# Kernel optimization log

Measured on AMD Instinct MI355X. Metric: run time of the kernel, lower is better.

The kernel has to match this reference:

```python
import jax, jax.numpy as jnp
import numpy as np

N, E = 20000, 320000
IN_DIM, HID, OUT_DIM, HEADS = 128, 64, 64, 4


def _lin_params(key, fan_in, fan_out):
    kw, kb = jax.random.split(key)
    s = 1.0 / np.sqrt(fan_in)
    W = jax.random.uniform(kw, (fan_in, fan_out), jnp.float32, -s, s)
    b = jax.random.uniform(kb, (fan_out,), jnp.float32, -s, s)
    return W, b


def setup_inputs() -> dict:
    key = jax.random.key(0)
    ks = jax.random.split(key, 12)
    x = jax.random.normal(ks[0], (N, IN_DIM), jnp.float32)
    edge_index = jax.random.randint(ks[1], (2, E), 0, N, jnp.int64)
    W1, b1 = _lin_params(ks[2], IN_DIM, HID)
    # conv1: in=HID, per-head out=HID, heads=HEADS, concat=True
    Wq1, bq1 = _lin_params(ks[3], HID, HID * HEADS)
    Wk1, bk1 = _lin_params(ks[4], HID, HID * HEADS)
    Wv1, bv1 = _lin_params(ks[5], HID, HID * HEADS)
    Ws1, bs1 = _lin_params(ks[6], HID, HID * HEADS)
    # conv2: in=HID*HEADS, out=OUT_DIM, heads=1, concat=False
    Wq2, bq2 = _lin_params(ks[7], HID * HEADS, OUT_DIM)
    Wk2, bk2 = _lin_params(ks[8], HID * HEADS, OUT_DIM)
    Wv2, bv2 = _lin_params(ks[9], HID * HEADS, OUT_DIM)
    Ws2, bs2 = _lin_params(ks[10], HID * HEADS, OUT_DIM)
    return dict(x=x, edge_index=edge_index, W1=W1, b1=b1,
                Wq1=Wq1, bq1=bq1, Wk1=Wk1, bk1=bk1, Wv1=Wv1, bv1=bv1, Ws1=Ws1, bs1=bs1,
                Wq2=Wq2, bq2=bq2, Wk2=Wk2, bk2=bk2, Wv2=Wv2, bv2=bv2, Ws2=Ws2, bs2=bs2)


def transformer_conv(x, src, dst, Wq, bq, Wk, bk, Wv, bv, Ws, bs, heads, concat):
    n = x.shape[0]
    c = Wq.shape[1] // heads  # per-head channels
    q = (x @ Wq + bq).reshape(n, heads, c)
    k = (x @ Wk + bk).reshape(n, heads, c)
    v = (x @ Wv + bv).reshape(n, heads, c)
    # per-edge attention logits, grouped-by-dst softmax
    alpha = jnp.einsum('ehc,ehc->eh', q[dst], k[src]) / jnp.sqrt(jnp.float32(c))
    m = jax.ops.segment_max(alpha, dst, num_segments=n)  # [n, heads]
    m = jnp.where(jnp.isfinite(m), m, 0.0)
    ex = jnp.exp(alpha - m[dst])
    denom = jax.ops.segment_sum(ex, dst, num_segments=n)
    a = ex / (denom[dst] + 1e-16)  # [E, heads]
    out = jax.ops.segment_sum(a[..., None] * v[src], dst, num_segments=n)  # [n, heads, c]
    out = out.reshape(n, heads * c) if concat else out.mean(axis=1)
    return out + (x @ Ws + bs)  # root/skip connection


def reference(x, edge_index, W1, b1, Wq1, bq1, Wk1, bk1, Wv1, bv1, Ws1, bs1,
              Wq2, bq2, Wk2, bk2, Wv2, bv2, Ws2, bs2):
    src, dst = edge_index[0], edge_index[1]
    h = jax.nn.relu(x @ W1 + b1)
    h = transformer_conv(h, src, dst, Wq1, bq1, Wk1, bk1, Wv1, bv1, Ws1, bs1, HEADS, True)
    h = jax.nn.relu(h)  # dropout is identity in eval mode
    out = transformer_conv(h, src, dst, Wq2, bq2, Wk2, bk2, Wv2, bv2, Ws2, bs2, 1, False)
    return out
```

## Files before the change

kernel.cpp:

```cpp
#include <hip/hip_runtime.h>
#include <hip/hip_bf16.h>
#include <math.h>

typedef short short8 __attribute__((ext_vector_type(8)));
typedef float f32x4 __attribute__((ext_vector_type(4)));
typedef float f32x2 __attribute__((ext_vector_type(2)));

__device__ __forceinline__ unsigned short pk_bf16(float x) {
    unsigned int b = __float_as_uint(x);
    b += 0x7fffu + ((b >> 16) & 1u);
    return (unsigned short)(b >> 16);
}
__device__ __forceinline__ void unpack8(const uint4 u, float* f) {
    f[0] = __uint_as_float(u.x << 16); f[1] = __uint_as_float(u.x & 0xffff0000u);
    f[2] = __uint_as_float(u.y << 16); f[3] = __uint_as_float(u.y & 0xffff0000u);
    f[4] = __uint_as_float(u.z << 16); f[5] = __uint_as_float(u.z & 0xffff0000u);
    f[6] = __uint_as_float(u.w << 16); f[7] = __uint_as_float(u.w & 0xffff0000u);
}
__device__ __forceinline__ unsigned char enc_fp8(float x) {
    return (unsigned char)(__builtin_amdgcn_cvt_pk_fp8_f32(x, x, 0, false) & 0xff);
}
__device__ __forceinline__ void unpack8_fp8(const uint2 u, float* f) {
    f32x2 a = __builtin_amdgcn_cvt_pk_f32_fp8(u.x, false);
    f32x2 b = __builtin_amdgcn_cvt_pk_f32_fp8(u.x, true);
    f32x2 c = __builtin_amdgcn_cvt_pk_f32_fp8(u.y, false);
    f32x2 d = __builtin_amdgcn_cvt_pk_f32_fp8(u.y, true);
    f[0] = a.x; f[1] = a.y; f[2] = b.x; f[3] = b.y;
    f[4] = c.x; f[5] = c.y; f[6] = d.x; f[7] = d.y;
}
__device__ __forceinline__ float qsum4(float x) {
    x += __int_as_float(__builtin_amdgcn_mov_dpp(__float_as_int(x), 0xB1, 0xF, 0xF, true));
    x += __int_as_float(__builtin_amdgcn_mov_dpp(__float_as_int(x), 0x4E, 0xF, 0xF, true));
    return x;
}

__global__ void count_kernel(const int* __restrict__ dst, int* __restrict__ deg, int E) {
    int e = blockIdx.x * blockDim.x + threadIdx.x;
    if (e < E) atomicAdd(&deg[dst[e]], 1);
}

__global__ __launch_bounds__(1024) void scanA_kernel(const int* __restrict__ deg,
                                                     int* __restrict__ offs,
                                                     int* __restrict__ bsum, int n) {
    __shared__ int s[1024];
    const int i = blockIdx.x * 1024 + threadIdx.x;
    const int v = (i < n) ? deg[i] : 0;
    s[threadIdx.x] = v;
    __syncthreads();
    for (int off = 1; off < 1024; off <<= 1) {
        int t = (threadIdx.x >= off) ? s[threadIdx.x - off] : 0;
        __syncthreads();
        s[threadIdx.x] += t;
        __syncthreads();
    }
    if (i < n) offs[i] = s[threadIdx.x] - v;
    if (threadIdx.x == 1023) bsum[blockIdx.x] = s[1023];
}

__global__ void scanB_kernel(const int* __restrict__ bsum, int* __restrict__ bpre, int nb) {
    const int t = threadIdx.x;
    int v = (t < nb) ? bsum[t] : 0;
    const int orig = v;
    for (int off = 1; off < 64; off <<= 1) {
        int o = __shfl_up(v, off, 64);
        if (t >= off) v += o;
    }
    if (t < nb) bpre[t] = v - orig;
    if (t == 63) bpre[nb] = v;
}

__global__ __launch_bounds__(1024) void scanC_kernel(int* __restrict__ offs,
                                                     int* __restrict__ cursor,
                                                     const int* __restrict__ bpre,
                                                     int n, int nb) {
    const int i = blockIdx.x * 1024 + threadIdx.x;
    if (i < n) {
        const int o = offs[i] + bpre[blockIdx.x];
        offs[i] = o;
        cursor[i] = o;
    }
    if (i == 0) offs[n] = bpre[nb];
}

__global__ void fill_kernel(const int* __restrict__ src, const int* __restrict__ dst,
                            int* __restrict__ cursor, int* __restrict__ csrc, int E) {
    int e = blockIdx.x * blockDim.x + threadIdx.x;
    if (e < E) {
        int p = atomicAdd(&cursor[dst[e]], 1);
        csrc[p] = src[e];
    }
}

template <int K, int NT, int CFG>
__device__ __forceinline__ void convw_body(const float* Wa, const float* Wb,
                                           const float* Wc, const float* Wd,
                                           unsigned short* out, int t) {
    constexpr int KS = K / 32;
    if (t >= NT * K * 64) return;
    const int jj = t & 7;
    const int lane = (t >> 3) & 63;
    const int nf = (t >> 9) & 3;
    const int rest = t >> 11;
    const int ks = rest % KS;
    const int nt = rest / KS;
    const int k = ks * 32 + (lane >> 4) * 8 + jj;
    const int c64 = nf * 16 + (lane & 15);
    float v;
    if (CFG == 1) {
        const int j = nt >> 2;
        const float* W = (j == 0) ? Wa : (j == 1) ? Wb : (j == 2) ? Wc : Wd;
        v = W[(size_t)k * 256 + (nt & 3) * 64 + c64];
    } else if (CFG == 2) {
        const float* W = (nt == 0) ? Wa : (nt == 1) ? Wb : (nt == 2) ? Wc : Wd;
        v = W[(size_t)k * 64 + c64];
    } else {
        v = Wa[(size_t)k * 64 + c64];
    }
    out[t] = pk_bf16(v);
}

__global__ __launch_bounds__(256) void prep_kernel(
    const float* __restrict__ x, unsigned short* __restrict__ xb, int nx, int nA,
    const float* __restrict__ W1, unsigned short* __restrict__ wswzL,
    const float* __restrict__ Wq1, const float* __restrict__ Wk1,
    const float* __restrict__ Wv1, const float* __restrict__ Ws1,
    unsigned short* __restrict__ wswz1,
    const float* __restrict__ Wq2, const float* __restrict__ Wk2,
    const float* __restrict__ Wv2, const float* __restrict__ Ws2,
    unsigned short* __restrict__ wswz2) {
    int b = blockIdx.x;
    if (b < nA) {
        int t = b * 256 + threadIdx.x;
        if (t < nx) xb[t] = pk_bf16(x[t]);
        return;
    }
    b -= nA;
    if (b < 32) { convw_body<128, 1, 0>(W1, W1, W1, W1, wswzL, b * 256 + threadIdx.x); return; }
    b -= 32;
    if (b < 256) { convw_body<64, 16, 1>(Wq1, Wk1, Wv1, Ws1, wswz1, b * 256 + threadIdx.x); return; }
    b -= 256;
    convw_body<256, 4, 2>(Wq2, Wk2, Wv2, Ws2, wswz2, b * 256 + threadIdx.x);
}

template <int K, int NT, int KIND>
__global__ __launch_bounds__(256) void mfma_gemm_kernel(
    const unsigned short* __restrict__ A, const unsigned short* __restrict__ Wswz,
    const float* __restrict__ ba, const float* __restrict__ bb,
    const float* __restrict__ bc, const float* __restrict__ bd,
    unsigned short* __restrict__ qout, unsigned char* __restrict__ kvout,
    void* __restrict__ sout, unsigned short* __restrict__ hout, int n) {
    constexpr int KS = K / 32;
    const int nt = blockIdx.x;
    const int w = threadIdx.x >> 6, l = threadIdx.x & 63;
    const int r0 = blockIdx.y * 64 + w * 16;
    const int lrow = l & 15, lk = l >> 4;

    f32x4 acc[4] = {};
    const unsigned short* wp = Wswz + (size_t)nt * KS * 4 * 512 + (size_t)l * 8;
    const unsigned short* ap = A + (size_t)(r0 + lrow) * K + lk * 8;

#pragma unroll
    for (int ks = 0; ks < KS; ++ks) {
        const short8 a = *(const short8*)(ap + ks * 32);
        const short8 b0 = *(const short8*)(wp + (ks * 4 + 0) * 512);
        const short8 b1 = *(const short8*)(wp + (ks * 4 + 1) * 512);
        const short8 b2 = *(const short8*)(wp + (ks * 4 + 2) * 512);
        const short8 b3 = *(const short8*)(wp + (ks * 4 + 3) * 512);
        acc[0] = __builtin_amdgcn_mfma_f32_16x16x32_bf16(a, b0, acc[0], 0, 0, 0);
        acc[1] = __builtin_amdgcn_mfma_f32_16x16x32_bf16(a, b1, acc[1], 0, 0, 0);
        acc[2] = __builtin_amdgcn_mfma_f32_16x16x32_bf16(a, b2, acc[2], 0, 0, 0);
        acc[3] = __builtin_amdgcn_mfma_f32_16x16x32_bf16(a, b3, acc[3], 0, 0, 0);
    }

    const int colg = l & 15, rowg = l >> 4;
#pragma unroll
    for (int nf = 0; nf < 4; ++nf) {
        const int c64 = nf * 16 + colg;
        float bias;
        if (KIND == 0) {
            bias = ba[c64];
        } else if (KIND == 1) {
            const int j = nt >> 2;
            const float* bsel = (j == 0) ? ba : (j == 1) ? bb : (j == 2) ? bc : bd;
            bias = bsel[(nt & 3) * 64 + c64];
        } else {
            const float* bsel = (nt == 0) ? ba : (nt == 1) ? bb : (nt == 2) ? bc : bd;
            bias = bsel[c64];
        }
#pragma unroll
        for (int r = 0; r < 4; ++r) {
            const int row = r0 + rowg * 4 + r;
            if (row >= n) continue;
            const float val = acc[nf][r] + bias;
            if (KIND == 0) {
                hout[(size_t)row * 64 + c64] = pk_bf16(fmaxf(val, 0.f));
            } else if (KIND == 1) {
                const int j = nt >> 2, hd = nt & 3;
                if (j == 0) {
                    qout[(size_t)row * 256 + hd * 64 + c64] = pk_bf16(val);
                } else if (j == 1) {
                    kvout[((size_t)row * 4 + hd) * 192 + c64] = enc_fp8(val);
                } else if (j == 2) {
                    *(unsigned short*)(kvout + ((size_t)row * 4 + hd) * 192 + 64 + c64 * 2) =
                        pk_bf16(val);
                } else {
                    ((unsigned short*)sout)[(size_t)row * 256 + hd * 64 + c64] = pk_bf16(val);
                }
            } else {
                if (nt == 0) {
                    qout[(size_t)row * 64 + c64] = pk_bf16(val);
                } else if (nt == 1) {
                    kvout[(size_t)row * 192 + c64] = enc_fp8(val);
                } else if (nt == 2) {
                    *(unsigned short*)(kvout + (size_t)row * 192 + 64 + c64 * 2) = pk_bf16(val);
                } else {
                    ((float*)sout)[(size_t)row * 64 + c64] = val;
                }
            }
        }
    }
}

__global__ __launch_bounds__(256) void attn4_kernel(
    const unsigned short* __restrict__ q, const unsigned char* __restrict__ kv,
    const unsigned short* __restrict__ s,
    const int* __restrict__ offs, const int* __restrict__ csrc,
    unsigned short* __restrict__ out, int n) {
    const int head = threadIdx.x >> 6;
    const int lane = threadIdx.x & 63;
    const int g = lane >> 3;
    const int sl = lane & 7;
    const int node = blockIdx.x;
    if (node >= n) return;
    const unsigned colbase = (head << 6) + (sl << 3);
    const unsigned koff = head * 192 + sl * 8;
    const unsigned voff = head * 192 + 64 + sl * 16;

    float qv[8];
    {
        uint4 qu = *(const uint4*)(q + ((unsigned)node << 8) + colbase);
        unpack8(qu, qv);
        const float qs = 0.125f * 1.44269504f;
#pragma unroll
        for (int i = 0; i < 8; ++i) qv[i] *= qs;
    }

    const int e0 = offs[node], e1 = offs[node + 1];
    float denom = 0.f;
    float acc[8] = {0.f, 0.f, 0.f, 0.f, 0.f, 0.f, 0.f, 0.f};

    int e = e0 + g;
    bool valid = e < e1;
    uint2 ku; uint4 vu;
    if (valid) {
        const unsigned char* kvp = kv + (size_t)(unsigned)csrc[e] * 768;
        ku = *(const uint2*)(kvp + koff);
        vu = *(const uint4*)(kvp + voff);
    }
    int en = e + 8;
    bool vn = en < e1;
    int srcn = vn ? csrc[en] : 0;

    while (valid) {
        uint2 kun; uint4 vun;
        if (vn) {
            const unsigned char* kvp = kv + (size_t)(unsigned)srcn * 768;
            kun = *(const uint2*)(kvp + koff);
            vun = *(const uint4*)(kvp + voff);
        }
        const int en2 = en + 8;
        const bool vn2 = en2 < e1;
        const int srcn2 = vn2 ? csrc[en2] : 0;

        float kf[8], vf[8];
        unpack8_fp8(ku, kf); unpack8(vu, vf);
        float dot = qv[0] * kf[0] + qv[1] * kf[1] + qv[2] * kf[2] + qv[3] * kf[3]
                  + qv[4] * kf[4] + qv[5] * kf[5] + qv[6] * kf[6] + qv[7] * kf[7];
        dot = qsum4(dot);
        dot += __shfl_xor(dot, 4, 64);
        const float wgt = __builtin_amdgcn_exp2f(dot);
#pragma unroll
        for (int i = 0; i < 8; ++i) acc[i] = fmaf(wgt, vf[i], acc[i]);
        denom += wgt;

        valid = vn; vn = vn2;
        en = en2; srcn = srcn2;
        ku = kun; vu = vun;
    }

#pragma unroll
    for (int off = 8; off <= 32; off <<= 1) {
        denom += __shfl_xor(denom, off, 64);
#pragma unroll
        for (int i = 0; i < 8; ++i) acc[i] += __shfl_xor(acc[i], off, 64);
    }

    if (g == 0) {
        float sv[8];
        uint4 su = *(const uint4*)(s + ((unsigned)node << 8) + colbase);
        unpack8(su, sv);
        const float inv = 1.f / (denom + 1e-16f);
        uint4 p;
        unsigned r[8];
#pragma unroll
        for (int i = 0; i < 8; ++i) r[i] = pk_bf16(fmaxf(acc[i] * inv + sv[i], 0.f));
        p.x = r[0] | (r[1] << 16);
        p.y = r[2] | (r[3] << 16);
        p.z = r[4] | (r[5] << 16);
        p.w = r[6] | (r[7] << 16);
        *(uint4*)(out + ((unsigned)node << 8) + colbase) = p;
    }
}

__global__ __launch_bounds__(256) void attn1_kernel(
    const unsigned short* __restrict__ q, const unsigned char* __restrict__ kv,
    const float* __restrict__ s,
    const int* __restrict__ offs, const int* __restrict__ csrc,
    float* __restrict__ out, int n) {
    const int w = threadIdx.x >> 6;
    const int lane = threadIdx.x & 63;
    const int g = lane >> 3;
    const int sl = lane & 7;
    const int node = blockIdx.x * 4 + w;
    if (node >= n) return;
    const unsigned koff = sl * 8;
    const unsigned voff = 64 + sl * 16;

    float qv[8];
    {
        uint4 qu = *(const uint4*)(q + ((unsigned)node << 6) + (sl << 3));
        unpack8(qu, qv);
        const float qs = 0.125f * 1.44269504f;
#pragma unroll
        for (int i = 0; i < 8; ++i) qv[i] *= qs;
    }

    const int e0 = offs[node], e1 = offs[node + 1];
    float denom = 0.f;
    float acc[8] = {0.f, 0.f, 0.f, 0.f, 0.f, 0.f, 0.f, 0.f};

    int e = e0 + g;
    bool valid = e < e1;
    uint2 ku; uint4 vu;
    if (valid) {
        const unsigned char* kvp = kv + (size_t)(unsigned)csrc[e] * 192;
        ku = *(const uint2*)(kvp + koff);
        vu = *(const uint4*)(kvp + voff);
    }
    int en = e + 8;
    bool vn = en < e1;
    int srcn = vn ? csrc[en] : 0;

    while (valid) {
        uint2 kun; uint4 vun;
        if (vn) {
            const unsigned char* kvp = kv + (size_t)(unsigned)srcn * 192;
            kun = *(const uint2*)(kvp + koff);
            vun = *(const uint4*)(kvp + voff);
        }
        const int en2 = en + 8;
        const bool vn2 = en2 < e1;
        const int srcn2 = vn2 ? csrc[en2] : 0;

        float kf[8], vf[8];
        unpack8_fp8(ku, kf); unpack8(vu, vf);
        float dot = qv[0] * kf[0] + qv[1] * kf[1] + qv[2] * kf[2] + qv[3] * kf[3]
                  + qv[4] * kf[4] + qv[5] * kf[5] + qv[6] * kf[6] + qv[7] * kf[7];
        dot = qsum4(dot);
        dot += __shfl_xor(dot, 4, 64);
        const float wgt = __builtin_amdgcn_exp2f(dot);
#pragma unroll
        for (int i = 0; i < 8; ++i) acc[i] = fmaf(wgt, vf[i], acc[i]);
        denom += wgt;

        valid = vn; vn = vn2;
        en = en2; srcn = srcn2;
        ku = kun; vu = vun;
    }

#pragma unroll
    for (int off = 8; off <= 32; off <<= 1) {
        denom += __shfl_xor(denom, off, 64);
#pragma unroll
        for (int i = 0; i < 8; ++i) acc[i] += __shfl_xor(acc[i], off, 64);
    }

    if (g == 0) {
        const float* sp = s + ((unsigned)node << 6) + (sl << 3);
        const float4 sva = *(const float4*)sp;
        const float4 svb = *(const float4*)(sp + 4);
        const float inv = 1.f / (denom + 1e-16f);
        float4 oa, ob;
        oa.x = acc[0] * inv + sva.x; oa.y = acc[1] * inv + sva.y;
        oa.z = acc[2] * inv + sva.z; oa.w = acc[3] * inv + sva.w;
        ob.x = acc[4] * inv + svb.x; ob.y = acc[5] * inv + svb.y;
        ob.z = acc[6] * inv + svb.z; ob.w = acc[7] * inv + svb.w;
        float* op = out + ((unsigned)node << 6) + (sl << 3);
        *(float4*)op = oa;
        *(float4*)(op + 4) = ob;
    }
}

extern "C" void kernel_launch(void* const* d_in, const int* in_sizes, int n_in,
                              void* d_out, int out_size, void* d_ws, size_t ws_size,
                              hipStream_t stream) {
    const float* x   = (const float*)d_in[0];
    const int*   ei  = (const int*)d_in[1];
    const float* W1  = (const float*)d_in[2];
    const float* b1  = (const float*)d_in[3];
    const float* Wq1 = (const float*)d_in[4];  const float* bq1 = (const float*)d_in[5];
    const float* Wk1 = (const float*)d_in[6];  const float* bk1 = (const float*)d_in[7];
    const float* Wv1 = (const float*)d_in[8];  const float* bv1 = (const float*)d_in[9];
    const float* Ws1 = (const float*)d_in[10]; const float* bs1 = (const float*)d_in[11];
    const float* Wq2 = (const float*)d_in[12]; const float* bq2 = (const float*)d_in[13];
    const float* Wk2 = (const float*)d_in[14]; const float* bk2 = (const float*)d_in[15];
    const float* Wv2 = (const float*)d_in[16]; const float* bv2 = (const float*)d_in[17];
    const float* Ws2 = (const float*)d_in[18]; const float* bs2 = (const float*)d_in[19];

    const int N = in_sizes[0] / 128;
    const int E = in_sizes[1] / 2;
    const int* srcv = ei;
    const int* dstv = ei + E;
    const int rowgroups = (N + 63) / 64;
    const int Mpad = rowgroups * 64;
    const int nscan = (N + 1023) / 1024;

    char* p = (char*)d_ws;
    auto alloc = [&](size_t bytes) -> void* {
        void* r = (void*)p;
        p += (bytes + 255) & ~(size_t)255;
        return r;
    };
    unsigned short* xb  = (unsigned short*)alloc((size_t)Mpad * 128 * 2);
    unsigned short* h1b = (unsigned short*)alloc((size_t)Mpad * 64 * 2);
    unsigned short* q1b = (unsigned short*)alloc((size_t)N * 256 * 2);
    unsigned char*  kv1 = (unsigned char*)alloc((size_t)N * 4 * 192);
    unsigned short* s1b = (unsigned short*)alloc((size_t)N * 256 * 2);
    unsigned short* h2b = (unsigned short*)alloc((size_t)Mpad * 256 * 2);
    unsigned short* q2b = (unsigned short*)alloc((size_t)N * 64 * 2);
    unsigned char*  kv2 = (unsigned char*)alloc((size_t)N * 192);
    float* s2 = (float*)alloc((size_t)N * 64 * 4);
    unsigned short* wswzL = (unsigned short*)alloc((size_t)1 * 128 * 64 * 2);
    unsigned short* wswz1 = (unsigned short*)alloc((size_t)16 * 64 * 64 * 2);
    unsigned short* wswz2 = (unsigned short*)alloc((size_t)4 * 256 * 64 * 2);
    int* deg    = (int*)alloc((size_t)N * 4);
    int* offs   = (int*)alloc(((size_t)N + 1) * 4);
    int* cursor = (int*)alloc((size_t)N * 4);
    int* csrc   = (int*)alloc((size_t)E * 4);
    int* bsum   = (int*)alloc((size_t)(nscan + 1) * 4);
    int* bpre   = (int*)alloc((size_t)(nscan + 1) * 4);
    (void)ws_size; (void)n_in; (void)out_size;

    hipMemsetAsync(deg, 0, (size_t)N * 4, stream);
    count_kernel<<<(E + 255) / 256, 256, 0, stream>>>(dstv, deg, E);
    scanA_kernel<<<nscan, 1024, 0, stream>>>(deg, offs, bsum, N);
    scanB_kernel<<<1, 64, 0, stream>>>(bsum, bpre, nscan);
    scanC_kernel<<<nscan, 1024, 0, stream>>>(offs, cursor, bpre, N, nscan);
    fill_kernel<<<(E + 255) / 256, 256, 0, stream>>>(srcv, dstv, cursor, csrc, E);

    const int nx = N * 128;
    const int nA = (nx + 255) / 256;
    prep_kernel<<<nA + 32 + 256 + 256, 256, 0, stream>>>(
        x, xb, nx, nA, W1, wswzL, Wq1, Wk1, Wv1, Ws1, wswz1, Wq2, Wk2, Wv2, Ws2, wswz2);

    mfma_gemm_kernel<128, 1, 0><<<dim3(1, rowgroups), 256, 0, stream>>>(
        xb, wswzL, b1, b1, b1, b1, nullptr, nullptr, nullptr, h1b, N);

    mfma_gemm_kernel<64, 16, 1><<<dim3(16, rowgroups), 256, 0, stream>>>(
        h1b, wswz1, bq1, bk1, bv1, bs1, q1b, kv1, (void*)s1b, nullptr, N);

    attn4_kernel<<<N, 256, 0, stream>>>(q1b, kv1, s1b, offs, csrc, h2b, N);

    mfma_gemm_kernel<256, 4, 2><<<dim3(4, rowgroups), 256, 0, stream>>>(
        h2b, wswz2, bq2, bk2, bv2, bs2, q2b, kv2, (void*)s2, nullptr, N);

    attn1_kernel<<<(N + 3) / 4, 256, 0, stream>>>(q2b, kv2, s2, offs, csrc,
                                                  (float*)d_out, N);
}
```

Measured before the change: 154.6 us.

## Fuse CSR-build kernels, merge first linear into fill, remap attn4 blocks by head

Folds the deg memset into the prep kernel and replaces the three-kernel scan with a single scan in which each block recomputes its prefix base by summing all earlier degrees. The first linear layer now runs inside the same launch as the CSR fill, which drops several launches and lets those two independent pieces of work overlap. attn4 now gives each block four nodes for one head, with blocks interleaved so that adjacent blocks cover the same head, which changes gather locality. The trade-off is redundant global reads of deg in the scan, since later blocks re-read nearly the whole array.

```diff
diff --git a/kernel.cpp b/kernel.cpp
--- a/kernel.cpp
+++ b/kernel.cpp
@@ -39,56 +39,38 @@
     if (e < E) atomicAdd(&deg[dst[e]], 1);
 }
 
-__global__ __launch_bounds__(1024) void scanA_kernel(const int* __restrict__ deg,
-                                                     int* __restrict__ offs,
-                                                     int* __restrict__ bsum, int n) {
+__global__ __launch_bounds__(1024) void scan_kernel(const int* __restrict__ deg,
+                                                    int* __restrict__ offs,
+                                                    int* __restrict__ cursor,
+                                                    int n, int nb) {
     __shared__ int s[1024];
-    const int i = blockIdx.x * 1024 + threadIdx.x;
+    const int b = blockIdx.x, t = threadIdx.x;
+    int partial = 0;
+    for (int i = t; i < b * 1024; i += 1024) partial += deg[i];
+    s[t] = partial;
+    __syncthreads();
+    for (int off = 512; off > 0; off >>= 1) {
+        if (t < off) s[t] += s[t + off];
+        __syncthreads();
+    }
+    const int base = s[0];
+    __syncthreads();
+    const int i = b * 1024 + t;
     const int v = (i < n) ? deg[i] : 0;
-    s[threadIdx.x] = v;
+    s[t] = v;
     __syncthreads();
     for (int off = 1; off < 1024; off <<= 1) {
-        int t = (threadIdx.x >= off) ? s[threadIdx.x - off] : 0;
+        int x = (t >= off) ? s[t - off] : 0;
         __syncthreads();
-        s[threadIdx.x] += t;
+        s[t] += x;
         __syncthreads();
     }
-    if (i < n) offs[i] = s[threadIdx.x] - v;
-    if (threadIdx.x == 1023) bsum[blockIdx.x] = s[1023];
-}
-
-__global__ void scanB_kernel(const int* __restrict__ bsum, int* __restrict__ bpre, int nb) {
-    const int t = threadIdx.x;
-    int v = (t < nb) ? bsum[t] : 0;
-    const int orig = v;
-    for (int off = 1; off < 64; off <<= 1) {
-        int o = __shfl_up(v, off, 64);
-        if (t >= off) v += o;
-    }
-    if (t < nb) bpre[t] = v - orig;
-    if (t == 63) bpre[nb] = v;
-}
-
-__global__ __launch_bounds__(1024) void scanC_kernel(int* __restrict__ offs,
-                                                     int* __restrict__ cursor,
-                                                     const int* __restrict__ bpre,
-                                                     int n, int nb) {
-    const int i = blockIdx.x * 1024 + threadIdx.x;
     if (i < n) {
-        const int o = offs[i] + bpre[blockIdx.x];
+        const int o = base + s[t] - v;
         offs[i] = o;
         cursor[i] = o;
     }
-    if (i == 0) offs[n] = bpre[nb];
-}
-
-__global__ void fill_kernel(const int* __restrict__ src, const int* __restrict__ dst,
-                            int* __restrict__ cursor, int* __restrict__ csrc, int E) {
-    int e = blockIdx.x * blockDim.x + threadIdx.x;
-    if (e < E) {
-        int p = atomicAdd(&cursor[dst[e]], 1);
-        csrc[p] = src[e];
-    }
+    if (b == nb - 1 && t == 1023) offs[n] = base + s[1023];
 }
 
 template <int K, int NT, int CFG>
@@ -127,7 +109,8 @@
     unsigned short* __restrict__ wswz1,
     const float* __restrict__ Wq2, const float* __restrict__ Wk2,
     const float* __restrict__ Wv2, const float* __restrict__ Ws2,
-    unsigned short* __restrict__ wswz2) {
+    unsigned short* __restrict__ wswz2,
+    int* __restrict__ deg, int ndeg) {
     int b = blockIdx.x;
     if (b < nA) {
         int t = b * 256 + threadIdx.x;
@@ -139,7 +122,12 @@
     b -= 32;
     if (b < 256) { convw_body<64, 16, 1>(Wq1, Wk1, Wv1, Ws1, wswz1, b * 256 + threadIdx.x); return; }
     b -= 256;
-    convw_body<256, 4, 2>(Wq2, Wk2, Wv2, Ws2, wswz2, b * 256 + threadIdx.x);
+    if (b < 256) { convw_body<256, 4, 2>(Wq2, Wk2, Wv2, Ws2, wswz2, b * 256 + threadIdx.x); return; }
+    b -= 256;
+    {
+        int t = b * 256 + threadIdx.x;
+        if (t < ndeg) deg[t] = 0;
+    }
 }
 
 template <int K, int NT, int KIND>
@@ -148,7 +136,7 @@
     const float* __restrict__ ba, const float* __restrict__ bb,
     const float* __restrict__ bc, const float* __restrict__ bd,
     unsigned short* __restrict__ qout, unsigned char* __restrict__ kvout,
-    void* __restrict__ sout, unsigned short* __restrict__ hout, int n) {
+    void* __restrict__ sout, int n) {
     constexpr int KS = K / 32;
     const int nt = blockIdx.x;
     const int w = threadIdx.x >> 6, l = threadIdx.x & 63;
@@ -177,9 +165,7 @@
     for (int nf = 0; nf < 4; ++nf) {
         const int c64 = nf * 16 + colg;
         float bias;
-        if (KIND == 0) {
-            bias = ba[c64];
-        } else if (KIND == 1) {
+        if (KIND == 1) {
             const int j = nt >> 2;
             const float* bsel = (j == 0) ? ba : (j == 1) ? bb : (j == 2) ? bc : bd;
             bias = bsel[(nt & 3) * 64 + c64];
@@ -192,9 +178,7 @@
             const int row = r0 + rowg * 4 + r;
             if (row >= n) continue;
             const float val = acc[nf][r] + bias;
-            if (KIND == 0) {
-                hout[(size_t)row * 64 + c64] = pk_bf16(fmaxf(val, 0.f));
-            } else if (KIND == 1) {
+            if (KIND == 1) {
                 const int j = nt >> 2, hd = nt & 3;
                 if (j == 0) {
                     qout[(size_t)row * 256 + hd * 64 + c64] = pk_bf16(val);
@@ -221,17 +205,75 @@
     }
 }
 
+__device__ __forceinline__ void lin_body(const unsigned short* __restrict__ A,
+                                         const unsigned short* __restrict__ Wswz,
+                                         const float* __restrict__ bias,
+                                         unsigned short* __restrict__ hout,
+                                         int n, int by, int tid) {
+    constexpr int K = 128, KS = 4;
+    const int w = tid >> 6, l = tid & 63;
+    const int r0 = by * 64 + w * 16;
+    const int lrow = l & 15, lk = l >> 4;
+
+    f32x4 acc[4] = {};
+    const unsigned short* wp = Wswz + (size_t)l * 8;
+    const unsigned short* ap = A + (size_t)(r0 + lrow) * K + lk * 8;
+
+#pragma unroll
+    for (int ks = 0; ks < KS; ++ks) {
+        const short8 a = *(const short8*)(ap + ks * 32);
+        const short8 b0 = *(const short8*)(wp + (ks * 4 + 0) * 512);
+        const short8 b1 = *(const short8*)(wp + (ks * 4 + 1) * 512);
+        const short8 b2 = *(const short8*)(wp + (ks * 4 + 2) * 512);
+        const short8 b3 = *(const short8*)(wp + (ks * 4 + 3) * 512);
+        acc[0] = __builtin_amdgcn_mfma_f32_16x16x32_bf16(a, b0, acc[0], 0, 0, 0);
+        acc[1] = __builtin_amdgcn_mfma_f32_16x16x32_bf16(a, b1, acc[1], 0, 0, 0);
+        acc[2] = __builtin_amdgcn_mfma_f32_16x16x32_bf16(a, b2, acc[2], 0, 0, 0);
+        acc[3] = __builtin_amdgcn_mfma_f32_16x16x32_bf16(a, b3, acc[3], 0, 0, 0);
+    }
+    const int colg = l & 15, rowg = l >> 4;
+#pragma unroll
+    for (int nf = 0; nf < 4; ++nf) {
+        const int c64 = nf * 16 + colg;
+        const float bias_v = bias[c64];
+#pragma unroll
+        for (int r = 0; r < 4; ++r) {
+            const int row = r0 + rowg * 4 + r;
+            if (row >= n) continue;
+            hout[(size_t)row * 64 + c64] = pk_bf16(fmaxf(acc[nf][r] + bias_v, 0.f));
+        }
+    }
+}
+
+__global__ __launch_bounds__(256) void fill_lin_kernel(
+    const int* __restrict__ src, const int* __restrict__ dst,
+    int* __restrict__ cursor, int* __restrict__ csrc, int E, int nfill,
+    const unsigned short* __restrict__ xb, const unsigned short* __restrict__ wswzL,
+    const float* __restrict__ b1, unsigned short* __restrict__ h1b, int n) {
+    if ((int)blockIdx.x < nfill) {
+        int e = blockIdx.x * 256 + threadIdx.x;
+        if (e < E) {
+            int p = atomicAdd(&cursor[dst[e]], 1);
+            csrc[p] = src[e];
+        }
+        return;
+    }
+    lin_body(xb, wswzL, b1, h1b, n, blockIdx.x - nfill, threadIdx.x);
+}
+
 __global__ __launch_bounds__(256) void attn4_kernel(
     const unsigned short* __restrict__ q, const unsigned char* __restrict__ kv,
     const unsigned short* __restrict__ s,
     const int* __restrict__ offs, const int* __restrict__ csrc,
     unsigned short* __restrict__ out, int n) {
-    const int head = threadIdx.x >> 6;
+    const int bid = blockIdx.x;
+    const int head = (bid & 7) >> 1;
+    const int ng = (bid >> 3) * 2 + (bid & 1);
     const int lane = threadIdx.x & 63;
+    const int node = ng * 4 + (threadIdx.x >> 6);
+    if (node >= n) return;
     const int g = lane >> 3;
     const int sl = lane & 7;
-    const int node = blockIdx.x;
-    if (node >= n) return;
     const unsigned colbase = (head << 6) + (sl << 3);
     const unsigned koff = head * 192 + sl * 8;
     const unsigned voff = head * 192 + 64 + sl * 16;
@@ -447,32 +489,32 @@
     int* offs   = (int*)alloc(((size_t)N + 1) * 4);
     int* cursor = (int*)alloc((size_t)N * 4);
     int* csrc   = (int*)alloc((size_t)E * 4);
-    int* bsum   = (int*)alloc((size_t)(nscan + 1) * 4);
-    int* bpre   = (int*)alloc((size_t)(nscan + 1) * 4);
     (void)ws_size; (void)n_in; (void)out_size;
-
-    hipMemsetAsync(deg, 0, (size_t)N * 4, stream);
-    count_kernel<<<(E + 255) / 256, 256, 0, stream>>>(dstv, deg, E);
-    scanA_kernel<<<nscan, 1024, 0, stream>>>(deg, offs, bsum, N);
-    scanB_kernel<<<1, 64, 0, stream>>>(bsum, bpre, nscan);
-    scanC_kernel<<<nscan, 1024, 0, stream>>>(offs, cursor, bpre, N, nscan);
-    fill_kernel<<<(E + 255) / 256, 256, 0, stream>>>(srcv, dstv, cursor, csrc, E);
 
     const int nx = N * 128;
     const int nA = (nx + 255) / 256;
-    prep_kernel<<<nA + 32 + 256 + 256, 256, 0, stream>>>(
-        x, xb, nx, nA, W1, wswzL, Wq1, Wk1, Wv1, Ws1, wswz1, Wq2, Wk2, Wv2, Ws2, wswz2);
-
-    mfma_gemm_kernel<128, 1, 0><<<dim3(1, rowgroups), 256, 0, stream>>>(
-        xb, wswzL, b1, b1, b1, b1, nullptr, nullptr, nullptr, h1b, N);
+    const int nZ = (N + 255) / 256;
+    prep_kernel<<<nA + 32 + 256 + 256 + nZ, 256, 0, stream>>>(
+        x, xb, nx, nA, W1, wswzL, Wq1, Wk1, Wv1, Ws1, wswz1,
+        Wq2, Wk2, Wv2, Ws2, wswz2, deg, N);
+
+    count_kernel<<<(E + 255) / 256, 256, 0, stream>>>(dstv, deg, E);
+
+    scan_kernel<<<nscan, 1024, 0, stream>>>(deg, offs, cursor, N, nscan);
+
+    const int nfill = (E + 255) / 256;
+    fill_lin_kernel<<<nfill + rowgroups, 256, 0, stream>>>(
+        srcv, dstv, cursor, csrc, E, nfill, xb, wswzL, b1, h1b, N);
 
     mfma_gemm_kernel<64, 16, 1><<<dim3(16, rowgroups), 256, 0, stream>>>(
-        h1b, wswz1, bq1, bk1, bv1, bs1, q1b, kv1, (void*)s1b, nullptr, N);
-
-    attn4_kernel<<<N, 256, 0, stream>>>(q1b, kv1, s1b, offs, csrc, h2b, N);
+        h1b, wswz1, bq1, bk1, bv1, bs1, q1b, kv1, (void*)s1b, N);
+
+    const int ngroups = (N + 3) / 4;
+    const int npairs = (ngroups + 1) / 2;
+    attn4_kernel<<<npairs * 8, 256, 0, stream>>>(q1b, kv1, s1b, offs, csrc, h2b, N);
 
     mfma_gemm_kernel<256, 4, 2><<<dim3(4, rowgroups), 256, 0, stream>>>(
-        h2b, wswz2, bq2, bk2, bv2, bs2, q2b, kv2, (void*)s2, nullptr, N);
+        h2b, wswz2, bq2, bk2, bv2, bs2, q2b, kv2, (void*)s2, N);
 
     attn1_kernel<<<(N + 3) / 4, 256, 0, stream>>>(q2b, kv2, s2, offs, csrc,
                                                   (float*)d_out, N);
```

Result: faster. 147.8 us (-4.4%).
